# Kernel tuning notes

Measured on AMD Instinct MI355X. Metric: run time of the kernel, lower is better.

The kernel has to match this reference:

```python
import jax, jax.numpy as jnp
import numpy as np

HEADS = 8
DIM_HEAD = 64
SCALE = DIM_HEAD ** -0.5
THRESH = 0.01


def setup_inputs() -> dict:
    key = jax.random.key(0)
    ks = jax.random.split(key, 5)
    b, n, dim = 4, 2048, 512
    inner = HEADS * DIM_HEAD  # 512
    x = jax.random.normal(ks[0], (b, n, dim), dtype=jnp.float32)
    Wqkv = jax.random.normal(ks[1], (dim, 3 * inner), dtype=jnp.float32) * (dim ** -0.5)
    bqkv = jax.random.normal(ks[2], (3 * inner,), dtype=jnp.float32) * 0.02
    Wout = jax.random.normal(ks[3], (inner, dim), dtype=jnp.float32) * (inner ** -0.5)
    bout = jax.random.normal(ks[4], (dim,), dtype=jnp.float32) * 0.02
    return {"x": x, "Wqkv": Wqkv, "bqkv": bqkv, "Wout": Wout, "bout": bout}


def reference(x, Wqkv, bqkv, Wout, bout):
    b, n, dim = x.shape
    qkv = x @ Wqkv + bqkv  # [b, n, 3*inner]
    q, k, v = jnp.split(qkv, 3, axis=-1)
    # b n (h d) -> b h n d
    split_heads = lambda t: t.reshape(b, n, HEADS, DIM_HEAD).transpose(0, 2, 1, 3)
    q, k, v = split_heads(q), split_heads(k), split_heads(v)
    dots = jnp.einsum('bhid,bhjd->bhij', q, k) * SCALE
    attn = jax.nn.softmax(dots, axis=-1)
    attn = jnp.where(attn > THRESH, attn, jnp.zeros_like(attn))
    out = jnp.einsum('bhij,bhjd->bhid', attn, v)
    out = out.transpose(0, 2, 1, 3).reshape(b, n, HEADS * DIM_HEAD)
    return out @ Wout + bout
```

## Files before the change

### kernel.cpp

```cpp
#include <hip/hip_runtime.h>

#define S_   2048
#define DM   512
#define HD   64
#define BHN  32

typedef unsigned short u16;
typedef __bf16 bf16x8 __attribute__((ext_vector_type(8)));
typedef float  f32x4  __attribute__((ext_vector_type(4)));

__device__ __forceinline__ float bf2f(u16 u) {
    union { unsigned int i; float f; } v; v.i = ((unsigned int)u) << 16; return v.f;
}
__device__ __forceinline__ u16 f2bf(float f) {
    union { float f; unsigned int i; } v; v.f = f;
    unsigned int i = v.i;
    return (u16)((i + 0x7FFFu + ((i >> 16) & 1u)) >> 16);
}
__device__ __forceinline__ void split3(float x, u16& b0, u16& b1, u16& b2) {
    b0 = f2bf(x);
    const float r0 = x - bf2f(b0);
    b1 = f2bf(r0);
    const float r1 = r0 - bf2f(b1);
    b2 = f2bf(r1);
}

__global__ __launch_bounds__(256) void prep_split_wT(
    const float* __restrict__ W, int N, int total,
    u16* __restrict__ w0, u16* __restrict__ w1, u16* __restrict__ w2)
{
    for (int idx = blockIdx.x * 256 + threadIdx.x; idx < total; idx += gridDim.x * 256) {
        const int n = idx >> 9, k = idx & 511;
        u16 a0, a1, a2;
        split3(W[(size_t)k * N + n], a0, a1, a2);
        w0[idx] = a0; w1[idx] = a1;
        if (w2) w2[idx] = a2;
    }
}

__global__ __launch_bounds__(256) void gemm_qkv_mfma(
    const float* __restrict__ A, const u16* __restrict__ Wt0, const u16* __restrict__ Wt1,
    const u16* __restrict__ Wt2, const float* __restrict__ bias,
    float* __restrict__ qh, float* __restrict__ kh, u16* __restrict__ vt)
{
    __shared__ __attribute__((aligned(16))) u16 As0[128 * 32], As1[128 * 32], As2[128 * 32];
    __shared__ __attribute__((aligned(16))) u16 Bs0[128 * 32], Bs1[128 * 32], Bs2[128 * 32];

    const int t  = threadIdx.x;
    const int m0 = blockIdx.y * 128, n0 = blockIdx.x * 128;
    const int w  = t >> 6, l = t & 63;
    const int wm = (w >> 1) * 64, wn = (w & 1) * 64;
    const int lr = l & 15, lq = l >> 4;

    const f32x4 zero4 = {0.f, 0.f, 0.f, 0.f};
    f32x4 acc[4][4];
#pragma unroll
    for (int i = 0; i < 4; i++)
#pragma unroll
        for (int j = 0; j < 4; j++) acc[i][j] = zero4;

    for (int k0 = 0; k0 < 512; k0 += 32) {
        __syncthreads();
#pragma unroll
        for (int i = 0; i < 4; i++) {
            const int e = t + 256 * i;
            const int r = e >> 3, c4 = (e & 7) * 4;
            const float4 f = *(const float4*)(&A[(size_t)(m0 + r) * 512 + k0 + c4]);
            const float xv[4] = {f.x, f.y, f.z, f.w};
            u16 a0[4], a1[4], a2[4];
#pragma unroll
            for (int j = 0; j < 4; j++) split3(xv[j], a0[j], a1[j], a2[j]);
            int2 p0, p1, p2;
            p0.x = a0[0] | (a0[1] << 16); p0.y = a0[2] | (a0[3] << 16);
            p1.x = a1[0] | (a1[1] << 16); p1.y = a1[2] | (a1[3] << 16);
            p2.x = a2[0] | (a2[1] << 16); p2.y = a2[2] | (a2[3] << 16);
            *(int2*)(&As0[r * 32 + c4]) = p0;
            *(int2*)(&As1[r * 32 + c4]) = p1;
            *(int2*)(&As2[r * 32 + c4]) = p2;
        }
#pragma unroll
        for (int i = 0; i < 2; i++) {
            const int e = t + 256 * i;
            const int r = e >> 2, c0 = (e & 3) * 8;
            *(int4*)(&Bs0[r * 32 + c0]) = *(const int4*)(&Wt0[(size_t)(n0 + r) * 512 + k0 + c0]);
            *(int4*)(&Bs1[r * 32 + c0]) = *(const int4*)(&Wt1[(size_t)(n0 + r) * 512 + k0 + c0]);
            *(int4*)(&Bs2[r * 32 + c0]) = *(const int4*)(&Wt2[(size_t)(n0 + r) * 512 + k0 + c0]);
        }
        __syncthreads();

#pragma unroll
        for (int i = 0; i < 4; i++) {
            const int ao = (wm + i * 16 + lr) * 32 + lq * 8;
            const bf16x8 a0 = *(const bf16x8*)(&As0[ao]);
            const bf16x8 a1 = *(const bf16x8*)(&As1[ao]);
            const bf16x8 a2 = *(const bf16x8*)(&As2[ao]);
#pragma unroll
            for (int j = 0; j < 4; j++) {
                const int bo = (wn + j * 16 + lr) * 32 + lq * 8;
                const bf16x8 b0 = *(const bf16x8*)(&Bs0[bo]);
                const bf16x8 b1 = *(const bf16x8*)(&Bs1[bo]);
                const bf16x8 b2 = *(const bf16x8*)(&Bs2[bo]);
                f32x4 c = acc[i][j];
                c = __builtin_amdgcn_mfma_f32_16x16x32_bf16(a0, b0, c, 0, 0, 0);
                c = __builtin_amdgcn_mfma_f32_16x16x32_bf16(a0, b1, c, 0, 0, 0);
                c = __builtin_amdgcn_mfma_f32_16x16x32_bf16(a1, b0, c, 0, 0, 0);
                c = __builtin_amdgcn_mfma_f32_16x16x32_bf16(a1, b1, c, 0, 0, 0);
                c = __builtin_amdgcn_mfma_f32_16x16x32_bf16(a0, b2, c, 0, 0, 0);
                c = __builtin_amdgcn_mfma_f32_16x16x32_bf16(a2, b0, c, 0, 0, 0);
                acc[i][j] = c;
            }
        }
    }

#pragma unroll
    for (int j = 0; j < 4; j++) {
        const int n = n0 + wn + j * 16 + lr;
        const float bv = bias[n];
        const int part = n >> 9, within = n & 511;
        const int h = within >> 6, d = within & 63;
#pragma unroll
        for (int i = 0; i < 4; i++) {
#pragma unroll
            for (int r = 0; r < 4; r++) {
                const int m = m0 + wm + i * 16 + lq * 4 + r;
                const int b = m >> 11, ns = m & 2047;
                const float val = acc[i][j][r] + bv;
                if (part == 0)
                    qh[(((size_t)(b * 8 + h)) * S_ + ns) * HD + d] = val;
                else if (part == 1)
                    kh[(((size_t)(b * 8 + h)) * S_ + ns) * HD + d] = val;
                else
                    vt[(((size_t)(b * 8 + h)) * HD + d) * S_ + ns] = f2bf(val);
            }
        }
    }
}

#define LDH 72

__global__ __launch_bounds__(256) void attn_mfma128(
    const float* __restrict__ q_ws, const float* __restrict__ k_ws,
    const u16* __restrict__ vt_ws, u16* __restrict__ ao_ws)
{
    __shared__ __attribute__((aligned(16))) u16 K0s[64 * LDH], K1s[64 * LDH], K2s[64 * LDH];
    __shared__ __attribute__((aligned(16))) u16 Vs[64 * LDH];
    __shared__ __attribute__((aligned(16))) u16 Ps[4][16 * LDH];

    const int t  = threadIdx.x;
    const int w  = t >> 6, l = t & 63;
    const int lr = l & 15, lq = l >> 4;
    const int bh = blockIdx.y, b = bh >> 3, h = bh & 7;
    const int q0 = blockIdx.x * 128;

    const float* qg  = q_ws + ((size_t)bh * S_ + q0) * HD;
    const float* kg0 = k_ws + (size_t)bh * S_ * HD;
    const u16*   vb  = vt_ws + (size_t)bh * HD * S_;

    bf16x8 fq0[2][2], fq1[2][2], fq2[2][2];
#pragma unroll
    for (int h2 = 0; h2 < 2; h2++) {
        __syncthreads();
#pragma unroll
        for (int i = 0; i < 4; i++) {
            const int e = t + 256 * i;
            const int row = e >> 4, c0 = (e & 15) * 4;
            const float4 f = *(const float4*)(qg + (size_t)h2 * 4096 + (size_t)e * 4);
            const float xv[4] = {f.x * 0.125f, f.y * 0.125f, f.z * 0.125f, f.w * 0.125f};
            u16 a0[4], a1[4], a2[4];
#pragma unroll
            for (int j = 0; j < 4; j++) split3(xv[j], a0[j], a1[j], a2[j]);
            int2 p0, p1, p2;
            p0.x = a0[0] | (a0[1] << 16); p0.y = a0[2] | (a0[3] << 16);
            p1.x = a1[0] | (a1[1] << 16); p1.y = a1[2] | (a1[3] << 16);
            p2.x = a2[0] | (a2[1] << 16); p2.y = a2[2] | (a2[3] << 16);
            *(int2*)(&K0s[row * LDH + c0]) = p0;
            *(int2*)(&K1s[row * LDH + c0]) = p1;
            *(int2*)(&K2s[row * LDH + c0]) = p2;
        }
        __syncthreads();
        if ((w >> 1) == h2) {
#pragma unroll
            for (int i = 0; i < 2; i++) {
#pragma unroll
                for (int kc = 0; kc < 2; kc++) {
                    const int o = ((w & 1) * 32 + i * 16 + lr) * LDH + kc * 32 + lq * 8;
                    fq0[i][kc] = *(const bf16x8*)(&K0s[o]);
                    fq1[i][kc] = *(const bf16x8*)(&K1s[o]);
                    fq2[i][kc] = *(const bf16x8*)(&K2s[o]);
                }
            }
        }
    }

    const f32x4 zero4 = {0.f, 0.f, 0.f, 0.f};
    double lsum[2][4];
#pragma unroll
    for (int i = 0; i < 2; i++)
#pragma unroll
        for (int r = 0; r < 4; r++) lsum[i][r] = 0.0;

    for (int jt = 0; jt < 32; jt++) {
        __syncthreads();
        const float* kg = kg0 + (size_t)jt * 64 * HD;
#pragma unroll
        for (int i = 0; i < 4; i++) {
            const int e = t + 256 * i;
            const int row = e >> 4, c0 = (e & 15) * 4;
            const float4 f = *(const float4*)(kg + (size_t)e * 4);
            const float xv[4] = {f.x, f.y, f.z, f.w};
            u16 a0[4], a1[4], a2[4];
#pragma unroll
            for (int j = 0; j < 4; j++) split3(xv[j], a0[j], a1[j], a2[j]);
            int2 p0, p1, p2;
            p0.x = a0[0] | (a0[1] << 16); p0.y = a0[2] | (a0[3] << 16);
            p1.x = a1[0] | (a1[1] << 16); p1.y = a1[2] | (a1[3] << 16);
            p2.x = a2[0] | (a2[1] << 16); p2.y = a2[2] | (a2[3] << 16);
            *(int2*)(&K0s[row * LDH + c0]) = p0;
            *(int2*)(&K1s[row * LDH + c0]) = p1;
            *(int2*)(&K2s[row * LDH + c0]) = p2;
        }
        __syncthreads();

#pragma unroll
        for (int i = 0; i < 2; i++) {
#pragma unroll
            for (int nt = 0; nt < 4; nt++) {
                f32x4 aHH = zero4, aC = zero4;
#pragma unroll
                for (int kc = 0; kc < 2; kc++) {
                    const int ko = (nt * 16 + lr) * LDH + kc * 32 + lq * 8;
                    const bf16x8 k0 = *(const bf16x8*)(&K0s[ko]);
                    const bf16x8 k1 = *(const bf16x8*)(&K1s[ko]);
                    const bf16x8 k2 = *(const bf16x8*)(&K2s[ko]);
                    aHH = __builtin_amdgcn_mfma_f32_16x16x32_bf16(fq0[i][kc], k0, aHH, 0, 0, 0);
                    aC  = __builtin_amdgcn_mfma_f32_16x16x32_bf16(fq0[i][kc], k1, aC, 0, 0, 0);
                    aC  = __builtin_amdgcn_mfma_f32_16x16x32_bf16(fq1[i][kc], k0, aC, 0, 0, 0);
                    aC  = __builtin_amdgcn_mfma_f32_16x16x32_bf16(fq1[i][kc], k1, aC, 0, 0, 0);
                    aC  = __builtin_amdgcn_mfma_f32_16x16x32_bf16(fq0[i][kc], k2, aC, 0, 0, 0);
                    aC  = __builtin_amdgcn_mfma_f32_16x16x32_bf16(fq2[i][kc], k0, aC, 0, 0, 0);
                }
#pragma unroll
                for (int r = 0; r < 4; r++) {
                    const float s = fminf(fmaxf(aHH[r] + aC[r], -30.f), 30.f);
                    lsum[i][r] += (double)__expf(s);
                }
            }
        }
    }
#pragma unroll
    for (int i = 0; i < 2; i++)
#pragma unroll
        for (int r = 0; r < 4; r++) {
#pragma unroll
            for (int off = 1; off < 16; off <<= 1)
                lsum[i][r] += __shfl_xor(lsum[i][r], off, 64);
        }
    double l_d[2][4]; float inv_l[2][4];
#pragma unroll
    for (int i = 0; i < 2; i++)
#pragma unroll
        for (int r = 0; r < 4; r++) {
            l_d[i][r] = lsum[i][r];
            inv_l[i][r] = (float)(1.0 / lsum[i][r]);
        }

    f32x4 oacc[2][4];
#pragma unroll
    for (int i = 0; i < 2; i++)
#pragma unroll
        for (int dt = 0; dt < 4; dt++) oacc[i][dt] = zero4;

    for (int jt = 0; jt < 32; jt++) {
        __syncthreads();
        const float* kg = kg0 + (size_t)jt * 64 * HD;
#pragma unroll
        for (int i = 0; i < 4; i++) {
            const int e = t + 256 * i;
            const int row = e >> 4, c0 = (e & 15) * 4;
            const float4 f = *(const float4*)(kg + (size_t)e * 4);
            int2 p0;
            p0.x = f2bf(f.x) | (f2bf(f.y) << 16);
            p0.y = f2bf(f.z) | (f2bf(f.w) << 16);
            *(int2*)(&K0s[row * LDH + c0]) = p0;
        }
#pragma unroll
        for (int i = 0; i < 2; i++) {
            const int e = t + 256 * i;
            const int row = e >> 3, c0 = (e & 7) * 8;
            *(int4*)(&Vs[row * LDH + c0]) = *(const int4*)(&vb[(size_t)row * S_ + jt * 64 + c0]);
        }
        __syncthreads();

#pragma unroll
        for (int i = 0; i < 2; i++) {
#pragma unroll
            for (int nt = 0; nt < 4; nt++) {
                f32x4 sacc = zero4;
#pragma unroll
                for (int kc = 0; kc < 2; kc++) {
                    const bf16x8 k0 = *(const bf16x8*)(&K0s[(nt * 16 + lr) * LDH + kc * 32 + lq * 8]);
                    sacc = __builtin_amdgcn_mfma_f32_16x16x32_bf16(fq0[i][kc], k0, sacc, 0, 0, 0);
                }
#pragma unroll
                for (int r = 0; r < 4; r++) {
                    const float s = fminf(fmaxf(sacc[r], -30.f), 30.f);
                    const float p = __expf(s) * inv_l[i][r];
                    u16 pb;
                    if (p > 0.0115f) {
                        pb = f2bf(p);
                    } else if (p < 0.009f) {
                        pb = 0;
                    } else {
                        const int row = q0 + w * 32 + i * 16 + lq * 4 + r;
                        const int col = jt * 64 + nt * 16 + lr;
                        const float* qr  = q_ws + ((size_t)bh * S_ + row) * HD;
                        const float* kcv = k_ws + ((size_t)bh * S_ + col) * HD;
                        double s64 = 0.0;
                        for (int d = 0; d < HD; d++) s64 += (double)qr[d] * (double)kcv[d];
                        s64 = fmin(fmax(s64 * 0.125, -30.0), 30.0);
                        const double pd = exp(s64) / l_d[i][r];
                        pb = (pd > 0.01) ? f2bf((float)pd) : (u16)0;
                    }
                    Ps[w][(lq * 4 + r) * LDH + nt * 16 + lr] = pb;
                }
            }
            __syncthreads();
#pragma unroll
            for (int kc = 0; kc < 2; kc++) {
                const bf16x8 ap = *(const bf16x8*)(&Ps[w][lr * LDH + kc * 32 + lq * 8]);
#pragma unroll
                for (int dt = 0; dt < 4; dt++) {
                    const bf16x8 bv = *(const bf16x8*)(&Vs[(dt * 16 + lr) * LDH + kc * 32 + lq * 8]);
                    oacc[i][dt] = __builtin_amdgcn_mfma_f32_16x16x32_bf16(ap, bv, oacc[i][dt], 0, 0, 0);
                }
            }
            __syncthreads();
        }
    }

#pragma unroll
    for (int i = 0; i < 2; i++)
#pragma unroll
        for (int dt = 0; dt < 4; dt++) {
#pragma unroll
            for (int r = 0; r < 4; r++) {
                const int row = q0 + w * 32 + i * 16 + lq * 4 + r;
                const int d   = dt * 16 + lr;
                ao_ws[((size_t)b * S_ + row) * DM + h * HD + d] = f2bf(oacc[i][dt][r]);
            }
        }
}

__global__ __launch_bounds__(256) void gemm_out_mfma(
    const u16* __restrict__ A, const u16* __restrict__ Wt0, const u16* __restrict__ Wt1,
    const float* __restrict__ bias, float* __restrict__ out)
{
    __shared__ __attribute__((aligned(16))) u16 As[128 * 32];
    __shared__ __attribute__((aligned(16))) u16 Bs0[128 * 32], Bs1[128 * 32];

    const int t  = threadIdx.x;
    const int m0 = blockIdx.y * 128, n0 = blockIdx.x * 128;
    const int w  = t >> 6, l = t & 63;
    const int wm = (w >> 1) * 64, wn = (w & 1) * 64;
    const int lr = l & 15, lq = l >> 4;

    const f32x4 zero4 = {0.f, 0.f, 0.f, 0.f};
    f32x4 acc[4][4];
#pragma unroll
    for (int i = 0; i < 4; i++)
#pragma unroll
        for (int j = 0; j < 4; j++) acc[i][j] = zero4;

    for (int k0 = 0; k0 < 512; k0 += 32) {
        __syncthreads();
#pragma unroll
        for (int i = 0; i < 2; i++) {
            const int e = t + 256 * i;
            const int r = e >> 2, c0 = (e & 3) * 8;
            *(int4*)(&As[r * 32 + c0])  = *(const int4*)(&A  [(size_t)(m0 + r) * 512 + k0 + c0]);
            *(int4*)(&Bs0[r * 32 + c0]) = *(const int4*)(&Wt0[(size_t)(n0 + r) * 512 + k0 + c0]);
            *(int4*)(&Bs1[r * 32 + c0]) = *(const int4*)(&Wt1[(size_t)(n0 + r) * 512 + k0 + c0]);
        }
        __syncthreads();

#pragma unroll
        for (int i = 0; i < 4; i++) {
            const bf16x8 a = *(const bf16x8*)(&As[(wm + i * 16 + lr) * 32 + lq * 8]);
#pragma unroll
            for (int j = 0; j < 4; j++) {
                const int bo = (wn + j * 16 + lr) * 32 + lq * 8;
                const bf16x8 b0 = *(const bf16x8*)(&Bs0[bo]);
                const bf16x8 b1 = *(const bf16x8*)(&Bs1[bo]);
                f32x4 c = acc[i][j];
                c = __builtin_amdgcn_mfma_f32_16x16x32_bf16(a, b0, c, 0, 0, 0);
                c = __builtin_amdgcn_mfma_f32_16x16x32_bf16(a, b1, c, 0, 0, 0);
                acc[i][j] = c;
            }
        }
    }

#pragma unroll
    for (int j = 0; j < 4; j++) {
        const int n = n0 + wn + j * 16 + lr;
        const float bv = bias[n];
#pragma unroll
        for (int i = 0; i < 4; i++) {
#pragma unroll
            for (int r = 0; r < 4; r++) {
                const int m = m0 + wm + i * 16 + lq * 4 + r;
                out[(size_t)m * 512 + n] = acc[i][j][r] + bv;
            }
        }
    }
}

extern "C" void kernel_launch(void* const* d_in, const int* in_sizes, int n_in,
                              void* d_out, int out_size, void* d_ws, size_t ws_size,
                              hipStream_t stream) {
    const float* x = nullptr; const float* Wqkv = nullptr; const float* bqkv = nullptr;
    const float* Wout = nullptr; const float* bout = nullptr;
    for (int i = 0; i < n_in; i++) {
        switch (in_sizes[i]) {
            case 4194304: x    = (const float*)d_in[i]; break;
            case 786432:  Wqkv = (const float*)d_in[i]; break;
            case 1536:    bqkv = (const float*)d_in[i]; break;
            case 262144:  Wout = (const float*)d_in[i]; break;
            case 512:     bout = (const float*)d_in[i]; break;
            default: break;
        }
    }
    if (!x)    x    = (const float*)d_in[0];
    if (!Wqkv) Wqkv = (const float*)d_in[1];
    if (!bqkv) bqkv = (const float*)d_in[2];
    if (!Wout) Wout = (const float*)d_in[3];
    if (!bout) bout = (const float*)d_in[4];

    float* out = (float*)d_out;

    char* ws = (char*)d_ws;
    float* q_ws  = (float*)(ws);
    float* k_ws  = (float*)(ws + (16ull << 20));
    u16* vt_ws = (u16*)(ws + (32ull << 20));
    u16* ao_ws = (u16*)(ws + (40ull << 20));
    u16* wt0 = (u16*)(ws + (40ull << 20));
    u16* wt1 = (u16*)(ws + (40ull << 20) + 1572864);
    u16* wt2 = (u16*)(ws + (40ull << 20) + 3145728);
    u16* wo0 = (u16*)(ws + (32ull << 20));
    u16* wo1 = (u16*)(ws + (32ull << 20) + 524288);

    prep_split_wT<<<3072, 256, 0, stream>>>(Wqkv, 1536, 1536 * 512, wt0, wt1, wt2);
    gemm_qkv_mfma<<<dim3(12, 64), 256, 0, stream>>>(
        x, wt0, wt1, wt2, bqkv, q_ws, k_ws, vt_ws);
    attn_mfma128<<<dim3(16, BHN), 256, 0, stream>>>(q_ws, k_ws, vt_ws, ao_ws);
    prep_split_wT<<<1024, 256, 0, stream>>>(Wout, 512, 512 * 512, wo0, wo1, nullptr);
    gemm_out_mfma<<<dim3(4, 64), 256, 0, stream>>>(ao_ws, wo0, wo1, bout, out);
}
```

Before: 509.9 us.

## Use two-term bf16 split for QK row-sum pass and wave-local LDS fences

The softmax normalizer pass now splits Q and K into two bf16 terms instead of three, cutting the MFMAs per tile from six to three and dropping one LDS buffer and one set of register fragments. Per-tile exponentials are accumulated in float and only then added to the double sums, removing most double-precision adds. The block-wide barriers around the per-wave P buffer are replaced by a wave-local lgkmcnt wait, since each wave only touches its own Ps slice. Risks are a less accurate row sum, which can move threshold decisions near 0.01, and possible ordering hazards if the Vs reuse depended on the removed barriers.

```diff
diff --git a/kernel.cpp b/kernel.cpp
--- a/kernel.cpp
+++ b/kernel.cpp
@@ -23,6 +23,14 @@
     b1 = f2bf(r0);
     const float r1 = r0 - bf2f(b1);
     b2 = f2bf(r1);
+}
+__device__ __forceinline__ void split2(float x, u16& b0, u16& b1) {
+    b0 = f2bf(x);
+    const float r0 = x - bf2f(b0);
+    b1 = f2bf(r0);
+}
+__device__ __forceinline__ void lds_fence_wave() {
+    asm volatile("s_waitcnt lgkmcnt(0)" ::: "memory");
 }
 
 __global__ __launch_bounds__(256) void prep_split_wT(
@@ -138,11 +146,11 @@
 
 #define LDH 72
 
-__global__ __launch_bounds__(256) void attn_mfma128(
+__global__ __launch_bounds__(256) void attn_v15(
     const float* __restrict__ q_ws, const float* __restrict__ k_ws,
     const u16* __restrict__ vt_ws, u16* __restrict__ ao_ws)
 {
-    __shared__ __attribute__((aligned(16))) u16 K0s[64 * LDH], K1s[64 * LDH], K2s[64 * LDH];
+    __shared__ __attribute__((aligned(16))) u16 K0s[64 * LDH], K1s[64 * LDH];
     __shared__ __attribute__((aligned(16))) u16 Vs[64 * LDH];
     __shared__ __attribute__((aligned(16))) u16 Ps[4][16 * LDH];
 
@@ -156,7 +164,7 @@
     const float* kg0 = k_ws + (size_t)bh * S_ * HD;
     const u16*   vb  = vt_ws + (size_t)bh * HD * S_;
 
-    bf16x8 fq0[2][2], fq1[2][2], fq2[2][2];
+    bf16x8 fq0[2][2], fq1[2][2];
 #pragma unroll
     for (int h2 = 0; h2 < 2; h2++) {
         __syncthreads();
@@ -166,16 +174,14 @@
             const int row = e >> 4, c0 = (e & 15) * 4;
             const float4 f = *(const float4*)(qg + (size_t)h2 * 4096 + (size_t)e * 4);
             const float xv[4] = {f.x * 0.125f, f.y * 0.125f, f.z * 0.125f, f.w * 0.125f};
-            u16 a0[4], a1[4], a2[4];
-#pragma unroll
-            for (int j = 0; j < 4; j++) split3(xv[j], a0[j], a1[j], a2[j]);
-            int2 p0, p1, p2;
+            u16 a0[4], a1[4];
+#pragma unroll
+            for (int j = 0; j < 4; j++) split2(xv[j], a0[j], a1[j]);
+            int2 p0, p1;
             p0.x = a0[0] | (a0[1] << 16); p0.y = a0[2] | (a0[3] << 16);
             p1.x = a1[0] | (a1[1] << 16); p1.y = a1[2] | (a1[3] << 16);
-            p2.x = a2[0] | (a2[1] << 16); p2.y = a2[2] | (a2[3] << 16);
             *(int2*)(&K0s[row * LDH + c0]) = p0;
             *(int2*)(&K1s[row * LDH + c0]) = p1;
-            *(int2*)(&K2s[row * LDH + c0]) = p2;
         }
         __syncthreads();
         if ((w >> 1) == h2) {
@@ -186,7 +192,6 @@
                     const int o = ((w & 1) * 32 + i * 16 + lr) * LDH + kc * 32 + lq * 8;
                     fq0[i][kc] = *(const bf16x8*)(&K0s[o]);
                     fq1[i][kc] = *(const bf16x8*)(&K1s[o]);
-                    fq2[i][kc] = *(const bf16x8*)(&K2s[o]);
                 }
             }
         }
@@ -208,18 +213,22 @@
             const int row = e >> 4, c0 = (e & 15) * 4;
             const float4 f = *(const float4*)(kg + (size_t)e * 4);
             const float xv[4] = {f.x, f.y, f.z, f.w};
-            u16 a0[4], a1[4], a2[4];
-#pragma unroll
-            for (int j = 0; j < 4; j++) split3(xv[j], a0[j], a1[j], a2[j]);
-            int2 p0, p1, p2;
+            u16 a0[4], a1[4];
+#pragma unroll
+            for (int j = 0; j < 4; j++) split2(xv[j], a0[j], a1[j]);
+            int2 p0, p1;
             p0.x = a0[0] | (a0[1] << 16); p0.y = a0[2] | (a0[3] << 16);
             p1.x = a1[0] | (a1[1] << 16); p1.y = a1[2] | (a1[3] << 16);
-            p2.x = a2[0] | (a2[1] << 16); p2.y = a2[2] | (a2[3] << 16);
             *(int2*)(&K0s[row * LDH + c0]) = p0;
             *(int2*)(&K1s[row * LDH + c0]) = p1;
-            *(int2*)(&K2s[row * LDH + c0]) = p2;
-        }
-        __syncthreads();
+        }
+        __syncthreads();
+
+        float esum[2][4];
+#pragma unroll
+        for (int i = 0; i < 2; i++)
+#pragma unroll
+            for (int r = 0; r < 4; r++) esum[i][r] = 0.f;
 
 #pragma unroll
         for (int i = 0; i < 2; i++) {
@@ -231,21 +240,21 @@
                     const int ko = (nt * 16 + lr) * LDH + kc * 32 + lq * 8;
                     const bf16x8 k0 = *(const bf16x8*)(&K0s[ko]);
                     const bf16x8 k1 = *(const bf16x8*)(&K1s[ko]);
-                    const bf16x8 k2 = *(const bf16x8*)(&K2s[ko]);
                     aHH = __builtin_amdgcn_mfma_f32_16x16x32_bf16(fq0[i][kc], k0, aHH, 0, 0, 0);
                     aC  = __builtin_amdgcn_mfma_f32_16x16x32_bf16(fq0[i][kc], k1, aC, 0, 0, 0);
                     aC  = __builtin_amdgcn_mfma_f32_16x16x32_bf16(fq1[i][kc], k0, aC, 0, 0, 0);
-                    aC  = __builtin_amdgcn_mfma_f32_16x16x32_bf16(fq1[i][kc], k1, aC, 0, 0, 0);
-                    aC  = __builtin_amdgcn_mfma_f32_16x16x32_bf16(fq0[i][kc], k2, aC, 0, 0, 0);
-                    aC  = __builtin_amdgcn_mfma_f32_16x16x32_bf16(fq2[i][kc], k0, aC, 0, 0, 0);
                 }
 #pragma unroll
                 for (int r = 0; r < 4; r++) {
                     const float s = fminf(fmaxf(aHH[r] + aC[r], -30.f), 30.f);
-                    lsum[i][r] += (double)__expf(s);
-                }
-            }
-        }
+                    esum[i][r] += __expf(s);
+                }
+            }
+        }
+#pragma unroll
+        for (int i = 0; i < 2; i++)
+#pragma unroll
+            for (int r = 0; r < 4; r++) lsum[i][r] += (double)esum[i][r];
     }
 #pragma unroll
     for (int i = 0; i < 2; i++)
@@ -324,7 +333,7 @@
                     Ps[w][(lq * 4 + r) * LDH + nt * 16 + lr] = pb;
                 }
             }
-            __syncthreads();
+            lds_fence_wave();
 #pragma unroll
             for (int kc = 0; kc < 2; kc++) {
                 const bf16x8 ap = *(const bf16x8*)(&Ps[w][lr * LDH + kc * 32 + lq * 8]);
@@ -334,7 +343,7 @@
                     oacc[i][dt] = __builtin_amdgcn_mfma_f32_16x16x32_bf16(ap, bv, oacc[i][dt], 0, 0, 0);
                 }
             }
-            __syncthreads();
+            lds_fence_wave();
         }
     }
 
@@ -451,7 +460,7 @@
     prep_split_wT<<<3072, 256, 0, stream>>>(Wqkv, 1536, 1536 * 512, wt0, wt1, wt2);
     gemm_qkv_mfma<<<dim3(12, 64), 256, 0, stream>>>(
         x, wt0, wt1, wt2, bqkv, q_ws, k_ws, vt_ws);
-    attn_mfma128<<<dim3(16, BHN), 256, 0, stream>>>(q_ws, k_ws, vt_ws, ao_ws);
+    attn_v15<<<dim3(16, BHN), 256, 0, stream>>>(q_ws, k_ws, vt_ws, ao_ws);
     prep_split_wT<<<1024, 256, 0, stream>>>(Wout, 512, 512 * 512, wo0, wo1, nullptr);
     gemm_out_mfma<<<dim3(4, 64), 256, 0, stream>>>(ao_ws, wo0, wo1, bout, out);
 }
```

Result: no change. 512.4 us (+0.5%).
